# Optimization experiments

Measured on AMD Instinct MI355X. Metric: run time of the kernel, lower is better.

## Reference

```python
import jax, jax.numpy as jnp
import numpy as np

EPS = 1e-12  # F.normalize eps


def setup_inputs() -> dict:
    key = jax.random.key(0)
    k1, k2, k3 = jax.random.split(key, 3)
    N, C, H, W, K = 64, 512, 28, 28, 64
    x = jax.random.normal(k1, (N, C, H, W), dtype=jnp.float32)
    conv_w = jax.random.normal(k2, (K, C), dtype=jnp.float32)  # 1x1 conv weight squeezed
    centroids = jax.random.uniform(k3, (K, C), dtype=jnp.float32)  # torch.rand init
    return {"x": x, "conv_w": conv_w, "centroids": centroids}


def reference(x, conv_w, centroids):
    N, C, H, W = x.shape
    K = centroids.shape[0]
    xf = x.reshape(N, C, H * W)                                  # (N, C, L)
    # 1x1 conv == matmul over channels, softmax over cluster dim
    logits = jnp.einsum('kc,ncl->nkl', conv_w, xf)               # (N, K, L)
    a = jax.nn.softmax(logits, axis=1)                           # softmax over clusters
    # vlad[n,k,c] = sum_l a[n,k,l] * (x[n,c,l] - cent[k,c])
    #            = (a @ x^T)[n,k,c] - (sum_l a[n,k,l]) * cent[k,c]
    agg = jnp.einsum('nkl,ncl->nkc', a, xf)                      # (N, K, C)
    vlad = agg - a.sum(axis=-1)[..., None] * centroids[None]     # (N, K, C)
    # intra-normalize per cluster (dim=2)
    vlad = vlad / jnp.maximum(jnp.linalg.norm(vlad, axis=2, keepdims=True), EPS)
    v = vlad.reshape(N, K * C)
    # global L2 normalize
    v = v / jnp.maximum(jnp.linalg.norm(v, axis=1, keepdims=True), EPS)
    return v
```

## Files before the change

### kernel.cpp

```cpp
#include <hip/hip_runtime.h>

#define C_ 512
#define L_ 784
#define K_ 64
#define EPS_ 1e-12f

typedef _Float16 half_t;
typedef _Float16 half4 __attribute__((ext_vector_type(4)));
typedef float float4v __attribute__((ext_vector_type(4)));

__global__ __launch_bounds__(1024) void kF(const float* __restrict__ x,
                                           const float* __restrict__ w,
                                           float* __restrict__ aggP,
                                           float* __restrict__ asumP) {
    __shared__ float  xs[2][32 * 256];
    __shared__ float  sl[16 * 64 * 4];
    __shared__ half_t ah[64 * 20];

    const int t    = threadIdx.x;
    const int n    = blockIdx.y;
    const int bx   = blockIdx.x;
    const int l0   = bx * 192;
    const int NT   = (bx == 3) ? 13 : 12;
    const int wv   = t >> 6;
    const int lane = t & 63;
    const int m16  = lane & 15;
    const int q    = lane >> 4;
    const int kt   = wv & 3;
    const int cs   = wv >> 2;

    const float* xn = x + (size_t)n * (C_ * L_);

    const int T0 = 2 * wv;
    const float* src0 = xn + (size_t)((T0 >> 3) * 128 + (T0 & 7) * 16 + m16) * L_ + l0 + 4 * q;
    const float* src1 = xn + (size_t)(((T0 + 1) >> 3) * 128 + ((T0 + 1) & 7) * 16 + m16) * L_ + l0 + 4 * q;

    {
        float4v g0 = *(const float4v*)src0;
        float4v g1 = *(const float4v*)src1;
        *(float4v*)&xs[0][T0 * 256 + lane * 4]       = g0;
        *(float4v*)&xs[0][(T0 + 1) * 256 + lane * 4] = g1;
    }

    half4 wf[8];
#pragma unroll
    for (int i = 0; i < 8; ++i) {
        float4v f = *(const float4v*)(w + (size_t)(kt * 16 + m16) * C_ +
                                      cs * 128 + i * 16 + 4 * q);
        wf[i] = half4{(half_t)f[0], (half_t)f[1], (half_t)f[2], (half_t)f[3]};
    }
    half4 ifr;
#pragma unroll
    for (int j = 0; j < 4; ++j) ifr[j] = (half_t)((4 * q + j == m16) ? 1.0f : 0.0f);

    const float4v z4 = {0.f, 0.f, 0.f, 0.f};
    float4v agc[8];
#pragma unroll
    for (int i = 0; i < 8; ++i) agc[i] = z4;
    float asum_reg = 0.f;

    __syncthreads();

    for (int s = 0; s < NT; ++s) {
        float4v g0, g1;
        const bool pf = (s + 1 < NT);
        if (pf) {
            g0 = *(const float4v*)(src0 + 16 * (s + 1));
            g1 = *(const float4v*)(src1 + 16 * (s + 1));
        }
        __builtin_amdgcn_sched_barrier(0);
        const float* xb = &xs[s & 1][(cs * 8) * 256];
        half4 bn[8];
        float4v lc[4] = {z4, z4, z4, z4};
#pragma unroll
        for (int i = 0; i < 8; ++i) {
            float4v f = *(const float4v*)&xb[i * 256 + lane * 4];
            bn[i] = half4{(half_t)f[0], (half_t)f[1], (half_t)f[2], (half_t)f[3]};
            float4v xt = __builtin_amdgcn_mfma_f32_16x16x16f16(bn[i], ifr, z4, 0, 0, 0);
            half4 a4 = {(half_t)xt[0], (half_t)xt[1], (half_t)xt[2], (half_t)xt[3]};
            lc[i & 3] = __builtin_amdgcn_mfma_f32_16x16x16f16(a4, wf[i], lc[i & 3], 0, 0, 0);
        }
        float4v lac = (lc[0] + lc[1]) + (lc[2] + lc[3]);
#pragma unroll
        for (int r = 0; r < 4; ++r)
            sl[((4 * q + r) * 64 + kt * 16 + m16) * 4 + cs] = lac[r];
        __syncthreads();
        {
            float4v p4 = *(const float4v*)&sl[(wv * 64 + lane) * 4];
            float lg = p4[0] + p4[1] + p4[2] + p4[3];
            float mx = lg;
#pragma unroll
            for (int off = 32; off; off >>= 1) mx = fmaxf(mx, __shfl_xor(mx, off, 64));
            float e = __expf(lg - mx);
            float sm = e;
#pragma unroll
            for (int off = 32; off; off >>= 1) sm += __shfl_xor(sm, off, 64);
            float a = e / sm;
            asum_reg += a;
            ah[lane * 20 + wv] = (half_t)a;
        }
        if (pf) {
            *(float4v*)&xs[(s + 1) & 1][T0 * 256 + lane * 4]       = g0;
            *(float4v*)&xs[(s + 1) & 1][(T0 + 1) * 256 + lane * 4] = g1;
        }
        __syncthreads();
        half4 aA = *(const half4*)&ah[(kt * 16 + m16) * 20 + 4 * q];
#pragma unroll
        for (int i = 0; i < 8; ++i)
            agc[i] = __builtin_amdgcn_mfma_f32_16x16x16f16(aA, bn[i], agc[i], 0, 0, 0);
    }

    sl[wv * 64 + lane] = asum_reg;
    __syncthreads();
    if (t < 64) {
        float s_ = 0.f;
#pragma unroll
        for (int j = 0; j < 16; ++j) s_ += sl[j * 64 + t];
        asumP[((size_t)n * 4 + bx) * 64 + t] = s_;
    }
    float* ap = aggP + (((size_t)n * 4 + bx) * 64) * (size_t)C_;
#pragma unroll
    for (int i = 0; i < 8; ++i)
#pragma unroll
        for (int r = 0; r < 4; ++r)
            ap[(size_t)(kt * 16 + 4 * q + r) * C_ + (cs * 8 + i) * 16 + m16] = agc[i][r];
}

__global__ __launch_bounds__(256) void kC(const float* __restrict__ aggP,
                                          const float* __restrict__ cent,
                                          const float* __restrict__ asumP,
                                          float* __restrict__ out) {
    __shared__ float asumS[4];
    const int t  = threadIdx.x;
    const int n  = blockIdx.y;
    const int k0 = blockIdx.x * 4;
    if (t < 4) {
        float s = 0.f;
        for (int j = 0; j < 4; ++j) s += asumP[((size_t)n * 4 + j) * 64 + k0 + t];
        asumS[t] = s;
    }
    __syncthreads();
    const int wv   = t >> 6;
    const int lane = t & 63;
    const int k    = k0 + wv;
    const float as = asumS[wv];
    const float* a0 = aggP + (((size_t)n * 4 + 0) * 64 + k) * C_;
    const float* a1 = aggP + (((size_t)n * 4 + 1) * 64 + k) * C_;
    const float* a2 = aggP + (((size_t)n * 4 + 2) * 64 + k) * C_;
    const float* a3 = aggP + (((size_t)n * 4 + 3) * 64 + k) * C_;
    const float* cp = cent + (size_t)k * C_;
    float4v v[2];
    float ss = 0.f;
#pragma unroll
    for (int j = 0; j < 2; ++j) {
        const int c = 4 * lane + 256 * j;
        float4v val = *(const float4v*)(a0 + c);
        val = val + *(const float4v*)(a1 + c);
        val = val + *(const float4v*)(a2 + c);
        val = val + *(const float4v*)(a3 + c);
        float4v c4 = *(const float4v*)(cp + c);
#pragma unroll
        for (int e = 0; e < 4; ++e) {
            val[e] -= as * c4[e];
            ss += val[e] * val[e];
        }
        v[j] = val;
    }
#pragma unroll
    for (int off = 32; off; off >>= 1) ss += __shfl_xor(ss, off, 64);
    const float scale = 1.f / (fmaxf(sqrtf(ss), EPS_) * 8.f);
    float* op = out + (size_t)n * (K_ * C_) + (size_t)k * C_;
#pragma unroll
    for (int j = 0; j < 2; ++j) {
        float4v o = v[j];
#pragma unroll
        for (int e = 0; e < 4; ++e) o[e] *= scale;
        *(float4v*)(op + 4 * lane + 256 * j) = o;
    }
}

extern "C" void kernel_launch(void* const* d_in, const int* in_sizes, int n_in,
                              void* d_out, int out_size, void* d_ws, size_t ws_size,
                              hipStream_t stream) {
    (void)in_sizes; (void)n_in; (void)out_size; (void)ws_size;
    const float* x    = (const float*)d_in[0];
    const float* w    = (const float*)d_in[1];
    const float* cent = (const float*)d_in[2];
    float* out = (float*)d_out;

    char* base = (char*)d_ws;
    float* aggP  = (float*)base;
    float* asumP = aggP + (size_t)64 * 4 * 64 * 512;

    kF<<<dim3(4, 64), 1024, 0, stream>>>(x, w, aggP, asumP);
    kC<<<dim3(16, 64), 256, 0, stream>>>(aggP, cent, asumP, out);
}
```

Measured before the change: 172.5 us.

## Split L across eight blocks and stage x tiles in LDS as fp16

The spatial dimension is now split into 8 chunks of 96 positions per batch element instead of 4 chunks of 192. This doubles the grid to 512 blocks so the GPU's compute units are better filled. The x tiles are converted to fp16 before they are written to shared memory, which halves LDS footprint and bandwidth and removes the per-iteration conversion after the read. In exchange, the partial aggregate workspace doubles, so the combine kernel must read and sum 8 partials per cluster instead of 4, adding global memory traffic.

```diff
diff --git a/kernel.cpp b/kernel.cpp
--- a/kernel.cpp
+++ b/kernel.cpp
@@ -9,19 +9,19 @@
 typedef _Float16 half4 __attribute__((ext_vector_type(4)));
 typedef float float4v __attribute__((ext_vector_type(4)));
 
-__global__ __launch_bounds__(1024) void kF(const float* __restrict__ x,
-                                           const float* __restrict__ w,
-                                           float* __restrict__ aggP,
-                                           float* __restrict__ asumP) {
-    __shared__ float  xs[2][32 * 256];
+__global__ __launch_bounds__(1024, 8) void kF(const float* __restrict__ x,
+                                              const float* __restrict__ w,
+                                              float* __restrict__ aggP,
+                                              float* __restrict__ asumP) {
+    __shared__ half_t xs[2][32 * 256];
     __shared__ float  sl[16 * 64 * 4];
     __shared__ half_t ah[64 * 20];
 
     const int t    = threadIdx.x;
     const int n    = blockIdx.y;
     const int bx   = blockIdx.x;
-    const int l0   = bx * 192;
-    const int NT   = (bx == 3) ? 13 : 12;
+    const int l0   = bx * 96;
+    const int NT   = (bx == 7) ? 7 : 6;
     const int wv   = t >> 6;
     const int lane = t & 63;
     const int m16  = lane & 15;
@@ -38,8 +38,10 @@
     {
         float4v g0 = *(const float4v*)src0;
         float4v g1 = *(const float4v*)src1;
-        *(float4v*)&xs[0][T0 * 256 + lane * 4]       = g0;
-        *(float4v*)&xs[0][(T0 + 1) * 256 + lane * 4] = g1;
+        *(half4*)&xs[0][T0 * 256 + lane * 4] =
+            half4{(half_t)g0[0], (half_t)g0[1], (half_t)g0[2], (half_t)g0[3]};
+        *(half4*)&xs[0][(T0 + 1) * 256 + lane * 4] =
+            half4{(half_t)g1[0], (half_t)g1[1], (half_t)g1[2], (half_t)g1[3]};
     }
 
     half4 wf[8];
@@ -69,13 +71,12 @@
             g1 = *(const float4v*)(src1 + 16 * (s + 1));
         }
         __builtin_amdgcn_sched_barrier(0);
-        const float* xb = &xs[s & 1][(cs * 8) * 256];
+        const half_t* xb = &xs[s & 1][(cs * 8) * 256];
         half4 bn[8];
         float4v lc[4] = {z4, z4, z4, z4};
 #pragma unroll
         for (int i = 0; i < 8; ++i) {
-            float4v f = *(const float4v*)&xb[i * 256 + lane * 4];
-            bn[i] = half4{(half_t)f[0], (half_t)f[1], (half_t)f[2], (half_t)f[3]};
+            bn[i] = *(const half4*)&xb[i * 256 + lane * 4];
             float4v xt = __builtin_amdgcn_mfma_f32_16x16x16f16(bn[i], ifr, z4, 0, 0, 0);
             half4 a4 = {(half_t)xt[0], (half_t)xt[1], (half_t)xt[2], (half_t)xt[3]};
             lc[i & 3] = __builtin_amdgcn_mfma_f32_16x16x16f16(a4, wf[i], lc[i & 3], 0, 0, 0);
@@ -100,8 +101,10 @@
             ah[lane * 20 + wv] = (half_t)a;
         }
         if (pf) {
-            *(float4v*)&xs[(s + 1) & 1][T0 * 256 + lane * 4]       = g0;
-            *(float4v*)&xs[(s + 1) & 1][(T0 + 1) * 256 + lane * 4] = g1;
+            *(half4*)&xs[(s + 1) & 1][T0 * 256 + lane * 4] =
+                half4{(half_t)g0[0], (half_t)g0[1], (half_t)g0[2], (half_t)g0[3]};
+            *(half4*)&xs[(s + 1) & 1][(T0 + 1) * 256 + lane * 4] =
+                half4{(half_t)g1[0], (half_t)g1[1], (half_t)g1[2], (half_t)g1[3]};
         }
         __syncthreads();
         half4 aA = *(const half4*)&ah[(kt * 16 + m16) * 20 + 4 * q];
@@ -116,9 +119,9 @@
         float s_ = 0.f;
 #pragma unroll
         for (int j = 0; j < 16; ++j) s_ += sl[j * 64 + t];
-        asumP[((size_t)n * 4 + bx) * 64 + t] = s_;
+        asumP[((size_t)n * 8 + bx) * 64 + t] = s_;
     }
-    float* ap = aggP + (((size_t)n * 4 + bx) * 64) * (size_t)C_;
+    float* ap = aggP + (((size_t)n * 8 + bx) * 64) * (size_t)C_;
 #pragma unroll
     for (int i = 0; i < 8; ++i)
 #pragma unroll
@@ -136,7 +139,7 @@
     const int k0 = blockIdx.x * 4;
     if (t < 4) {
         float s = 0.f;
-        for (int j = 0; j < 4; ++j) s += asumP[((size_t)n * 4 + j) * 64 + k0 + t];
+        for (int j = 0; j < 8; ++j) s += asumP[((size_t)n * 8 + j) * 64 + k0 + t];
         asumS[t] = s;
     }
     __syncthreads();
@@ -144,20 +147,17 @@
     const int lane = t & 63;
     const int k    = k0 + wv;
     const float as = asumS[wv];
-    const float* a0 = aggP + (((size_t)n * 4 + 0) * 64 + k) * C_;
-    const float* a1 = aggP + (((size_t)n * 4 + 1) * 64 + k) * C_;
-    const float* a2 = aggP + (((size_t)n * 4 + 2) * 64 + k) * C_;
-    const float* a3 = aggP + (((size_t)n * 4 + 3) * 64 + k) * C_;
+    const float* ab = aggP + ((size_t)n * 8 * 64 + k) * C_;
     const float* cp = cent + (size_t)k * C_;
     float4v v[2];
     float ss = 0.f;
 #pragma unroll
     for (int j = 0; j < 2; ++j) {
         const int c = 4 * lane + 256 * j;
-        float4v val = *(const float4v*)(a0 + c);
-        val = val + *(const float4v*)(a1 + c);
-        val = val + *(const float4v*)(a2 + c);
-        val = val + *(const float4v*)(a3 + c);
+        float4v val = {0.f, 0.f, 0.f, 0.f};
+#pragma unroll
+        for (int p = 0; p < 8; ++p)
+            val = val + *(const float4v*)(ab + (size_t)p * 64 * C_ + c);
         float4v c4 = *(const float4v*)(cp + c);
 #pragma unroll
         for (int e = 0; e < 4; ++e) {
@@ -190,8 +190,8 @@
 
     char* base = (char*)d_ws;
     float* aggP  = (float*)base;
-    float* asumP = aggP + (size_t)64 * 4 * 64 * 512;
+    float* asumP = aggP + (size_t)64 * 8 * 64 * 512;
 
-    kF<<<dim3(4, 64), 1024, 0, stream>>>(x, w, aggP, asumP);
+    kF<<<dim3(8, 64), 1024, 0, stream>>>(x, w, aggP, asumP);
     kC<<<dim3(16, 64), 256, 0, stream>>>(aggP, cent, asumP, out);
 }
```

After: 352.8 us. 2.05x slower.
